# Optimization experiments

Hardware: AMD Instinct MI355X
Metric: run time of the kernel (lower is better)

The kernel has to match this reference:

```python
import jax, jax.numpy as jnp
import numpy as np

EPS = 1e-5
P = 3  # p_size
BW = 1.0  # bandwidth


def _instance_norm(x):
    # calc_mean_std: per (B,C) mean/std over spatial dims, unbiased var (torch default)
    b, c, h, w = x.shape
    flat = x.reshape(b, c, h * w)
    mean = flat.mean(-1)[:, :, None, None]
    std = jnp.sqrt(flat.var(-1, ddof=1) + EPS)[:, :, None, None]
    return (x - mean) / std


def _conv1x1(x, w, bias):
    # x: (B,C,H,W), w: (O,C), bias: (O,)
    return jnp.einsum('oc,bchw->bohw', w, x) + bias[None, :, None, None]


def _patches_scaled(x, scale):
    # ReflectionPad2d(1) + Unfold(3) -> (B, HW, C*9), torch layout (c slow, k fast),
    # with ContextAtten scale applied over the 9 kernel positions.
    b, c, h, w = x.shape
    pad = jnp.pad(x, ((0, 0), (0, 0), (1, 1), (1, 1)), mode='reflect')
    # (B,C,H,W,9)
    p9 = jnp.stack([pad[:, :, di:di + h, dj:dj + w]
                    for di in range(P) for dj in range(P)], axis=-1)
    p9 = p9 * scale  # broadcast over last (kernel) axis
    # -> (B,H,W,C,9) -> (B, HW, C*9)
    return p9.transpose(0, 2, 3, 1, 4).reshape(b, h * w, c * P * P)


def setup_inputs() -> dict:
    key = jax.random.key(0)
    ks = jax.random.split(key, 12)
    B, C, H, W = 2, 512, 64, 64
    IC = 256
    f32 = jnp.float32
    inp = {
        'content': jax.random.normal(ks[0], (B, C, H, W), f32),
        'style': jax.random.normal(ks[1], (B, C, H, W), f32),
        'fusion_style': jax.random.normal(ks[2], (B, C, H, W), f32),
        'theta_w': jax.random.normal(ks[3], (IC, C), f32) * np.sqrt(2.0 / C),
        'theta_b': jnp.zeros((IC,), f32),
        'phi_w': jax.random.normal(ks[4], (IC, C), f32) * np.sqrt(2.0 / C),
        'phi_b': jnp.zeros((IC,), f32),
        'g_w': jax.random.normal(ks[5], (IC, C), f32) * np.sqrt(2.0 / C),
        'g_b': jnp.zeros((IC,), f32),
        'W_w': jax.random.normal(ks[6], (C, IC), f32) * np.sqrt(2.0 / IC),
        'W_b': jnp.zeros((C,), f32),
        'scale': jnp.ones((P * P,), f32),
    }
    return inp


def reference(content, style, fusion_style, theta_w, theta_b, phi_w, phi_b,
              g_w, g_b, W_w, W_b, scale):
    B, C, H, W = content.shape
    IC = theta_w.shape[0]
    HW = H * W

    # g on fusion_style -> (B, HW, IC)
    g_s = _conv1x1(fusion_style, g_w, g_b).reshape(B, IC, HW).transpose(0, 2, 1)

    # instance-normalize content/style (normal=True path)
    xn = _instance_norm(content)
    sn = _instance_norm(style)

    theta_x = _conv1x1(xn, theta_w, theta_b)
    phi_s = _conv1x1(sn, phi_w, phi_b)

    theta_p = _patches_scaled(theta_x, scale)  # (B, HW, IC*9)
    phi_p = _patches_scaled(phi_s, scale)      # (B, HW, IC*9)

    f = jnp.einsum('blk,bmk->blm', theta_p, phi_p) * BW  # (B, HW, HW)
    f_div_C = jax.nn.softmax(f, axis=-1)

    y = jnp.einsum('blm,bmo->blo', f_div_C, g_s)  # (B, HW, IC)
    y = y.transpose(0, 2, 1).reshape(B, IC, H, W)
    W_y = _conv1x1(y, W_w, W_b)  # (B, C, H, W)
    # isTraining=True path: conf_map = 0
    return W_y
```

## Files before the change

### kernel.cpp

```cpp
#include <hip/hip_runtime.h>
#include <stdint.h>

typedef __attribute__((ext_vector_type(8))) __bf16 bf16x8;
typedef __attribute__((ext_vector_type(4))) float f32x4;
typedef __attribute__((ext_vector_type(4))) unsigned int uint4v;

__device__ __forceinline__ float bf2f(unsigned short u){
  unsigned int x = ((unsigned int)u) << 16;
  return __builtin_bit_cast(float, x);
}
__device__ __forceinline__ unsigned short f2bf(float f){
  unsigned int x = __builtin_bit_cast(unsigned int, f);
  x += 0x7FFFu + ((x >> 16) & 1u);
  return (unsigned short)(x >> 16);
}

#define OUT_PART 4
#define OUT_PARTH 5

template<int OM>
__global__ __launch_bounds__(256)
void gemm_bt(const unsigned short* __restrict__ A, int lda,
             const unsigned short* __restrict__ Bt, int ldb,
             int kchunk, void* __restrict__ Out, int ldo,
             size_t zStride, size_t aBatch, size_t bBatch,
             int sMask, int sShift)
{
  __shared__ uint4v AsmBuf[1024];
  __shared__ uint4v BsmBuf[1024];
  char* Asm = (char*)AsmBuf;
  char* Bsm = (char*)BsmBuf;

  const int tid  = threadIdx.x;
  const int lane = tid & 63;
  const int wave = tid >> 6;
  const int wy = wave >> 1, wx = wave & 1;
  const int lm = lane & 15, quad = lane >> 4;
  const int tileM = blockIdx.y * 128;
  const int tileN = blockIdx.x * 128;
  const int z = blockIdx.z;
  const int slice = z & sMask;
  const int batch = z >> sShift;

  A  += (size_t)slice*kchunk + (size_t)batch*aBatch;
  Bt += (size_t)slice*kchunk + (size_t)batch*bBatch;

  const int sr0 = tid >> 2, sc0 = tid & 3;
  const int sr1 = sr0 + 64;
  const size_t gA0 = (size_t)(tileM + sr0)*lda + ((sc0 ^ ((sr0 >> 1) & 3)) << 3);
  const size_t gA1 = (size_t)(tileM + sr1)*lda + ((sc0 ^ ((sr1 >> 1) & 3)) << 3);
  const size_t gB0 = (size_t)(tileN + sr0)*ldb + ((sc0 ^ ((sr0 >> 1) & 3)) << 3);
  const size_t gB1 = (size_t)(tileN + sr1)*ldb + ((sc0 ^ ((sr1 >> 1) & 3)) << 3);
  const int lOff0 = sr0*64 + sc0*16;
  const int lOff1 = sr1*64 + sc0*16;

  int aOff[4], bOff[4];
#pragma unroll
  for (int t = 0; t < 4; ++t){
    int ra = wy*64 + t*16 + lm;
    aOff[t] = ra*64 + ((quad ^ ((ra >> 1) & 3)) << 4);
    int rb = wx*64 + t*16 + lm;
    bOff[t] = rb*64 + ((quad ^ ((rb >> 1) & 3)) << 4);
  }

  f32x4 acc[4][4] = {};

  const int ksteps = kchunk >> 5;
  uint4v a0v = *(const uint4v*)(A + gA0);
  uint4v a1v = *(const uint4v*)(A + gA1);
  uint4v b0v = *(const uint4v*)(Bt + gB0);
  uint4v b1v = *(const uint4v*)(Bt + gB1);

  for (int kt = 0; kt < ksteps; ++kt){
    char* As = Asm + (kt & 1)*8192;
    char* Bs = Bsm + (kt & 1)*8192;
    *(uint4v*)(As + lOff0) = a0v;
    *(uint4v*)(As + lOff1) = a1v;
    *(uint4v*)(Bs + lOff0) = b0v;
    *(uint4v*)(Bs + lOff1) = b1v;
    __syncthreads();
    if (kt + 1 < ksteps){
      const unsigned short* Ak = A + (kt + 1)*32;
      const unsigned short* Bk = Bt + (kt + 1)*32;
      a0v = *(const uint4v*)(Ak + gA0);
      a1v = *(const uint4v*)(Ak + gA1);
      b0v = *(const uint4v*)(Bk + gB0);
      b1v = *(const uint4v*)(Bk + gB1);
    }
    bf16x8 af[4], bfr[4];
#pragma unroll
    for (int t = 0; t < 4; ++t){
      af[t]  = __builtin_bit_cast(bf16x8, *(const uint4v*)(As + aOff[t]));
      bfr[t] = __builtin_bit_cast(bf16x8, *(const uint4v*)(Bs + bOff[t]));
    }
#pragma unroll
    for (int tm = 0; tm < 4; ++tm)
#pragma unroll
      for (int tn = 0; tn < 4; ++tn)
        acc[tm][tn] = __builtin_amdgcn_mfma_f32_16x16x32_bf16(af[tm], bfr[tn], acc[tm][tn], 0, 0, 0);
  }

#pragma unroll
  for (int tm = 0; tm < 4; ++tm){
    const int rowb = tileM + wy*64 + tm*16 + quad*4;
#pragma unroll
    for (int tn = 0; tn < 4; ++tn){
      const int col = tileN + wx*64 + tn*16 + lm;
#pragma unroll
      for (int r = 0; r < 4; ++r){
        const float v = acc[tm][tn][r];
        const size_t idx = (size_t)z*zStride + (size_t)(rowb + r)*ldo + col;
        if (OM == OUT_PART) ((float*)Out)[idx] = v;
        else                ((unsigned short*)Out)[idx] = f2bf(v);
      }
    }
  }
}

template<int OM>
__global__ __launch_bounds__(256)
void gemm_wide(const unsigned short* __restrict__ A, int lda,
               const unsigned short* __restrict__ Bt, int ldb,
               int kchunk, void* __restrict__ Out, int ldo,
               size_t zStride, size_t aBatch, size_t bBatch,
               int sMask, int sShift)
{
  __shared__ uint4v AsmBuf[1024];
  __shared__ uint4v BsmBuf[2048];
  char* Asm = (char*)AsmBuf;
  char* Bsm = (char*)BsmBuf;

  const int tid  = threadIdx.x;
  const int lane = tid & 63;
  const int wave = tid >> 6;
  const int wy = wave >> 1, wx = wave & 1;
  const int lm = lane & 15, quad = lane >> 4;
  const int tileM = blockIdx.y * 128;
  const int tileN = blockIdx.x * 256;
  const int z = blockIdx.z;
  const int slice = z & sMask;
  const int batch = z >> sShift;

  A  += (size_t)slice*kchunk + (size_t)batch*aBatch;
  Bt += (size_t)slice*kchunk + (size_t)batch*bBatch;

  const int sr = tid >> 2, sc = tid & 3;
  size_t gA[2]; int lA[2];
  size_t gB[4]; int lB[4];
#pragma unroll
  for (int i = 0; i < 2; ++i){
    const int r = sr + 64*i;
    gA[i] = (size_t)(tileM + r)*lda + ((sc ^ ((r >> 1) & 3)) << 3);
    lA[i] = r*64 + sc*16;
  }
#pragma unroll
  for (int i = 0; i < 4; ++i){
    const int r = sr + 64*i;
    gB[i] = (size_t)(tileN + r)*ldb + ((sc ^ ((r >> 1) & 3)) << 3);
    lB[i] = r*64 + sc*16;
  }

  int aOff[4], bOff[8];
#pragma unroll
  for (int t = 0; t < 4; ++t){
    const int ra = wy*64 + t*16 + lm;
    aOff[t] = ra*64 + ((quad ^ ((ra >> 1) & 3)) << 4);
  }
#pragma unroll
  for (int t = 0; t < 8; ++t){
    const int rb = wx*128 + t*16 + lm;
    bOff[t] = rb*64 + ((quad ^ ((rb >> 1) & 3)) << 4);
  }

  f32x4 acc[4][8] = {};

  const int ksteps = kchunk >> 5;
  uint4v av[2], bv[4];
#pragma unroll
  for (int i = 0; i < 2; ++i) av[i] = *(const uint4v*)(A + gA[i]);
#pragma unroll
  for (int i = 0; i < 4; ++i) bv[i] = *(const uint4v*)(Bt + gB[i]);

  for (int kt = 0; kt < ksteps; ++kt){
    char* As = Asm + (kt & 1)*8192;
    char* Bs = Bsm + (kt & 1)*16384;
#pragma unroll
    for (int i = 0; i < 2; ++i) *(uint4v*)(As + lA[i]) = av[i];
#pragma unroll
    for (int i = 0; i < 4; ++i) *(uint4v*)(Bs + lB[i]) = bv[i];
    __syncthreads();
    if (kt + 1 < ksteps){
      const unsigned short* Ak = A + (kt + 1)*32;
      const unsigned short* Bk = Bt + (kt + 1)*32;
#pragma unroll
      for (int i = 0; i < 2; ++i) av[i] = *(const uint4v*)(Ak + gA[i]);
#pragma unroll
      for (int i = 0; i < 4; ++i) bv[i] = *(const uint4v*)(Bk + gB[i]);
    }
    bf16x8 af[4], bfr[8];
#pragma unroll
    for (int t = 0; t < 4; ++t)
      af[t] = __builtin_bit_cast(bf16x8, *(const uint4v*)(As + aOff[t]));
#pragma unroll
    for (int t = 0; t < 8; ++t)
      bfr[t] = __builtin_bit_cast(bf16x8, *(const uint4v*)(Bs + bOff[t]));
#pragma unroll
    for (int tm = 0; tm < 4; ++tm)
#pragma unroll
      for (int tn = 0; tn < 8; ++tn)
        acc[tm][tn] = __builtin_amdgcn_mfma_f32_16x16x32_bf16(af[tm], bfr[tn], acc[tm][tn], 0, 0, 0);
  }

#pragma unroll
  for (int tm = 0; tm < 4; ++tm){
    const int rowb = tileM + wy*64 + tm*16 + quad*4;
#pragma unroll
    for (int tn = 0; tn < 8; ++tn){
      const int col = tileN + wx*128 + tn*16 + lm;
#pragma unroll
      for (int r = 0; r < 4; ++r){
        const float v = acc[tm][tn][r];
        const size_t idx = (size_t)z*zStride + (size_t)(rowb + r)*ldo + col;
        if (OM == OUT_PART) ((float*)Out)[idx] = v;
        else                ((unsigned short*)Out)[idx] = f2bf(v);
      }
    }
  }
}

typedef const __attribute__((address_space(1))) unsigned int* gas1_t;
typedef __attribute__((address_space(3))) unsigned int* las3_t;
__device__ __forceinline__ void gload16(const void* g, void* l){
  __builtin_amdgcn_global_load_lds((gas1_t)g, (las3_t)l, 16, 0, 0);
}

__global__ __launch_bounds__(512)
void gemm_big256(const unsigned short* __restrict__ A, int lda,
                 const unsigned short* __restrict__ Bt, int ldb,
                 int K, float* __restrict__ Out, int ldo,
                 size_t aBatch, size_t bBatch, size_t oBatch)
{
  __shared__ char lds[65536];

  const int tid  = threadIdx.x;
  const int lane = tid & 63;
  const int wv   = tid >> 6;
  const int wy = wv >> 2, wx = wv & 3;
  const int lm = lane & 15, quad = lane >> 4;
  const int tileM = blockIdx.y * 256;
  const int tileN = blockIdx.x * 256;
  const int z = blockIdx.z;

  A   += (size_t)z*aBatch;
  Bt  += (size_t)z*bBatch;
  Out += (size_t)z*oBatch;

  const int srow  = tid >> 2;
  const int selem = (((tid & 3) ^ ((tid >> 3) & 3)) << 3);
  const size_t gAs  = (size_t)(tileM + srow)*lda + selem;
  const size_t gAs2 = gAs + (size_t)128*lda;
  const size_t gBs  = (size_t)(tileN + srow)*ldb + selem;
  const size_t gBs2 = gBs + (size_t)128*ldb;
  const int ldsSt = tid << 4;

  const int xq    = (quad ^ ((lm >> 1) & 3)) << 4;
  const int aBase = (wy*128 + lm)*64 + xq;
  const int bBase = (wx*64  + lm)*64 + xq;

  f32x4 acc[8][4] = {};
  const int nk = K >> 5;

  gload16(A  + gAs,  lds + ldsSt);
  gload16(A  + gAs2, lds + ldsSt + 8192);
  gload16(Bt + gBs,  lds + 16384 + ldsSt);
  gload16(Bt + gBs2, lds + 16384 + ldsSt + 8192);

  for (int kt = 0; kt < nk; ++kt){
    if (kt + 1 < nk){
      char* nbuf = lds + ((kt + 1) & 1)*32768;
      const unsigned short* Ak = A  + (kt + 1)*32;
      const unsigned short* Bk = Bt + (kt + 1)*32;
      gload16(Ak + gAs,  nbuf + ldsSt);
      gload16(Ak + gAs2, nbuf + ldsSt + 8192);
      gload16(Bk + gBs,  nbuf + 16384 + ldsSt);
      gload16(Bk + gBs2, nbuf + 16384 + ldsSt + 8192);
      asm volatile("s_waitcnt vmcnt(4)" ::: "memory");
    } else {
      asm volatile("s_waitcnt vmcnt(0)" ::: "memory");
    }
    __builtin_amdgcn_s_barrier();
    __builtin_amdgcn_sched_barrier(0);

    const char* As = lds + (kt & 1)*32768;
    const char* Bs = As + 16384;

    bf16x8 a[4], b[4];
#pragma unroll
    for (int n = 0; n < 4; ++n)
      b[n] = __builtin_bit_cast(bf16x8, *(const uint4v*)(Bs + bBase + n*1024));
#pragma unroll
    for (int m = 0; m < 4; ++m)
      a[m] = __builtin_bit_cast(bf16x8, *(const uint4v*)(As + aBase + m*1024));

    __builtin_amdgcn_s_barrier();
    __builtin_amdgcn_s_setprio(1);
#pragma unroll
    for (int m = 0; m < 4; ++m)
#pragma unroll
      for (int n = 0; n < 4; ++n)
        acc[m][n] = __builtin_amdgcn_mfma_f32_16x16x32_bf16(a[m], b[n], acc[m][n], 0, 0, 0);
    __builtin_amdgcn_s_setprio(0);
    __builtin_amdgcn_s_barrier();
    __builtin_amdgcn_sched_barrier(0);

#pragma unroll
    for (int m = 0; m < 4; ++m)
      a[m] = __builtin_bit_cast(bf16x8, *(const uint4v*)(As + aBase + (m + 4)*1024));
    __builtin_amdgcn_s_setprio(1);
#pragma unroll
    for (int m = 0; m < 4; ++m)
#pragma unroll
      for (int n = 0; n < 4; ++n)
        acc[m + 4][n] = __builtin_amdgcn_mfma_f32_16x16x32_bf16(a[m], b[n], acc[m + 4][n], 0, 0, 0);
    __builtin_amdgcn_s_setprio(0);
    __builtin_amdgcn_sched_barrier(0);
    __builtin_amdgcn_s_barrier();
    __builtin_amdgcn_sched_barrier(0);
    asm volatile("" ::: "memory");
  }

#pragma unroll
  for (int tm = 0; tm < 8; ++tm){
    const int rowb = tileM + wy*128 + tm*16 + quad*4;
#pragma unroll
    for (int tn = 0; tn < 4; ++tn){
      const int col = tileN + wx*64 + tn*16 + lm;
#pragma unroll
      for (int r = 0; r < 4; ++r)
        Out[(size_t)(rowb + r)*ldo + col] = acc[tm][tn][r];
    }
  }
}

__global__ __launch_bounds__(256)
void reduce_tp(const float* __restrict__ part,
               const float* __restrict__ tb, const float* __restrict__ pb,
               unsigned short* __restrict__ th, unsigned short* __restrict__ ph)
{
  const size_t i = (size_t)blockIdx.x*256 + threadIdx.x;
  const int which = (int)(i >> 21);
  const size_t j = i & 0x1FFFFFu;
  const int col = (int)(j & 255u);
  float v = 0.f;
#pragma unroll
  for (int s = 0; s < 4; ++s)
    v += part[(size_t)((which << 2) + s)*2097152 + j];
  v += (which ? pb : tb)[col];
  unsigned short hi = f2bf(v);
  unsigned short lo = f2bf(v - bf2f(hi));
  const size_t o = (j >> 8)*768 + col;
  unsigned short* O = which ? ph : th;
  const int dup = which ? 512 : 256;
  const int loo = which ? 256 : 512;
  O[o] = hi; O[o + dup] = hi; O[o + loo] = lo;
}

__global__ __launch_bounds__(256)
void reduce_g(const unsigned short* __restrict__ part,
              const float* __restrict__ gb, unsigned short* __restrict__ gs)
{
  const size_t i = (size_t)blockIdx.x*256 + threadIdx.x;
  float v = 0.f;
#pragma unroll
  for (int s = 0; s < 4; ++s) v += bf2f(part[(size_t)s*2097152 + i]);
  gs[i] = f2bf(v + gb[i >> 13]);
}

__global__ __launch_bounds__(256)
void reduce_y(const unsigned short* __restrict__ part,
              unsigned short* __restrict__ yb)
{
  const size_t i = (size_t)blockIdx.x*256 + threadIdx.x;
  const int b = (int)(i >> 20);
  const size_t j = i & 0xFFFFFu;
  float v = 0.f;
#pragma unroll
  for (int s = 0; s < 8; ++s)
    v += bf2f(part[(size_t)((b << 3) + s)*1048576 + j]);
  yb[i] = f2bf(v);
}

__global__ __launch_bounds__(256)
void reduce_w(const float* __restrict__ part, const float* __restrict__ wb,
              void* __restrict__ Out, const unsigned int* __restrict__ flagPtr)
{
  const size_t i = (size_t)blockIdx.x*256 + threadIdx.x;
  const int b = (int)(i >> 21);
  const size_t j = i & 0x1FFFFFu;
  float v = part[(size_t)(b << 1)*2097152 + j]
          + part[(size_t)((b << 1) | 1)*2097152 + j]
          + wb[(i >> 12) & 511u];
  if (flagPtr[0]) ((float*)Out)[i] = v;
  else            ((unsigned short*)Out)[i] = f2bf(v);
}

__global__ __launch_bounds__(256)
void detect_prep(const void* __restrict__ content,
                 const void* tb, const void* pb, const void* gb, const void* wb,
                 const void* sc,
                 unsigned int* __restrict__ flag, float* __restrict__ scale_c,
                 float* tb_c, float* pb_c, float* gb_c, float* wb_c)
{
  __shared__ int cnt;
  __shared__ unsigned int flg;
  const int tid = threadIdx.x;
  if (tid == 0) cnt = 0;
  __syncthreads();
  unsigned int w = ((const unsigned int*)content)[tid];
  int e = (w >> 23) & 0xFF;
  if (e >= 0x70 && e <= 0x8F) atomicAdd(&cnt, 1);
  __syncthreads();
  if (tid == 0){ flg = (cnt >= 128) ? 1u : 0u; flag[0] = flg; }
  __syncthreads();
  const unsigned int f = flg;
  auto rd = [&](const void* p, int i)->float{
    return f ? ((const float*)p)[i] : bf2f(((const unsigned short*)p)[i]);
  };
  if (tid < 9) scale_c[tid] = rd(sc, tid);
  tb_c[tid] = rd(tb, tid);
  pb_c[tid] = rd(pb, tid);
  gb_c[tid] = rd(gb, tid);
  wb_c[tid] = rd(wb, tid);
  wb_c[tid + 256] = rd(wb, tid + 256);
}

__global__ __launch_bounds__(256)
void conv_weights(const void* tw, const void* pw, const void* gw, const void* www,
                  const unsigned int* __restrict__ flagPtr,
                  unsigned short* __restrict__ wdup,
                  unsigned short* __restrict__ gwc,
                  unsigned short* __restrict__ wwc)
{
  const unsigned int fl = flagPtr[0];
  const int sec = blockIdx.y;
  const int idx = blockIdx.x*256 + threadIdx.x;
  auto rd = [&](const void* p, int i)->float{
    return fl ? ((const float*)p)[i] : bf2f(((const unsigned short*)p)[i]);
  };
  if (sec < 2){
    const void* w = sec ? pw : tw;
    const int o = idx >> 9, c = idx & 511;
    float v = rd(w, o*512 + c);
    unsigned short hi = f2bf(v);
    unsigned short lo = f2bf(v - bf2f(hi));
    unsigned short* base = wdup + (size_t)sec*256*1536 + o*1536;
    base[c] = hi; base[512 + c] = lo; base[1024 + c] = hi;
  } else if (sec == 2){
    const int o = idx >> 9, c = idx & 511;
    gwc[o*512 + c] = f2bf(rd(gw, o*512 + c));
  } else {
    const int o = idx >> 8, c = idx & 255;
    wwc[o*256 + c] = f2bf(rd(www, o*256 + c));
  }
}

__global__ __launch_bounds__(256)
void stats_all(const void* __restrict__ content, const void* __restrict__ style,
               const unsigned int* __restrict__ flagPtr,
               float* __restrict__ statsC, float* __restrict__ statsS)
{
  const unsigned int fl = flagPtr[0];
  const void* X = blockIdx.z ? style : content;
  float* stats = blockIdx.z ? statsS : statsC;
  const int bc = blockIdx.x;
  const int tid = threadIdx.x;
  float s = 0.f, q = 0.f;
  if (fl){
    const f32x4* row = (const f32x4*)((const float*)X + (size_t)bc*4096);
#pragma unroll
    for (int i = 0; i < 4; ++i){
      f32x4 v = row[tid + i*256];
#pragma unroll
      for (int j = 0; j < 4; ++j){ s += v[j]; q += v[j]*v[j]; }
    }
  } else {
    const uint4v* row = (const uint4v*)((const unsigned short*)X + (size_t)bc*4096);
#pragma unroll
    for (int i = 0; i < 2; ++i){
      uint4v u = row[tid + i*256];
#pragma unroll
      for (int j = 0; j < 4; ++j){
        float a = bf2f((unsigned short)(u[j] & 0xffffu));
        float b = bf2f((unsigned short)(u[j] >> 16));
        s += a + b; q += a*a + b*b;
      }
    }
  }
#pragma unroll
  for (int off = 32; off > 0; off >>= 1){
    s += __shfl_down(s, off);
    q += __shfl_down(q, off);
  }
  __shared__ float rs[4], rq[4];
  if ((tid & 63) == 0){ rs[tid >> 6] = s; rq[tid >> 6] = q; }
  __syncthreads();
  if (tid == 0){
    s = rs[0] + rs[1] + rs[2] + rs[3];
    q = rq[0] + rq[1] + rq[2] + rq[3];
    float mean = s * (1.0f/4096.0f);
    float var  = (q - 4096.0f*mean*mean) * (1.0f/4095.0f);
    stats[bc*2 + 0] = mean;
    stats[bc*2 + 1] = 1.0f / sqrtf(var + 1e-5f);
  }
}

__global__ __launch_bounds__(256)
void norm_all(const void* __restrict__ content, const void* __restrict__ style,
              const void* __restrict__ fusion,
              const float* __restrict__ statsC, const float* __restrict__ statsS,
              unsigned short* __restrict__ xn, unsigned short* __restrict__ sn,
              unsigned short* __restrict__ fst,
              const unsigned int* __restrict__ flagPtr)
{
  __shared__ float tile[64][65];
  const unsigned int fl = flagPtr[0];
  const int z = blockIdx.z;
  const int which = z >> 1;
  const int b  = z & 1;
  const int l0 = blockIdx.x * 64;
  const int c0 = blockIdx.y * 64;
  const int tid = threadIdx.x;
  const int tx = tid & 63, ty = tid >> 6;

  const void* X = which == 0 ? content : (which == 1 ? style : fusion);
#pragma unroll
  for (int p = 0; p < 16; ++p){
    const int cc = ty + p*4;
    const size_t src = ((size_t)b*512 + c0 + cc)*4096 + l0 + tx;
    tile[cc][tx] = fl ? ((const float*)X)[src]
                      : bf2f(((const unsigned short*)X)[src]);
  }
  __syncthreads();
  if (which < 2){
    const float* stats = which ? statsS : statsC;
    const float mean = stats[(b*512 + c0 + tx)*2 + 0];
    const float inv  = stats[(b*512 + c0 + tx)*2 + 1];
    unsigned short* Out = which ? sn : xn;
#pragma unroll
    for (int p = 0; p < 16; ++p){
      const int lj = ty + p*4;
      const float v = (tile[tx][lj] - mean) * inv;
      const size_t o = ((size_t)b*4096 + l0 + lj)*1536 + c0 + tx;
      const unsigned short hi = f2bf(v);
      Out[o] = hi;
      Out[o + 512] = hi;
      Out[o + 1024] = f2bf(v - bf2f(hi));
    }
  } else {
#pragma unroll
    for (int p = 0; p < 16; ++p){
      const int lj = ty + p*4;
      const size_t o = ((size_t)b*4096 + l0 + lj)*512 + c0 + tx;
      fst[o] = f2bf(tile[tx][lj]);
    }
  }
}

__global__ __launch_bounds__(256)
void softmax_rows(const float* __restrict__ Gbase, const float* __restrict__ scale_c,
                  unsigned short* __restrict__ Pbase)
{
  const int bb = blockIdx.x >> 12;
  const int l  = blockIdx.x & 4095;
  const float* G = Gbase + (size_t)bb*16777216;
  unsigned short* P = Pbase + (size_t)bb*16777216;
  const int yy = l >> 6, xx = l & 63;
  const int tid = threadIdx.x;

  float s2[9];
  const float* rowp[9];
#pragma unroll
  for (int di = 0; di < 3; ++di){
    int ry = yy + di - 1; ry = ry < 0 ? 1 : (ry > 63 ? 62 : ry);
#pragma unroll
    for (int dj = 0; dj < 3; ++dj){
      int rx = xx + dj - 1; rx = rx < 0 ? 1 : (rx > 63 ? 62 : rx);
      const int k = di*3 + dj;
      const float s = scale_c[k];
      s2[k] = s*s;
      rowp[k] = G + (size_t)(ry*64 + rx)*4096;
    }
  }

  float fv[16];
  float mx = -3.0e38f;
#pragma unroll
  for (int i = 0; i < 16; ++i){
    const int m = tid + i*256;
    const int my = m >> 6, mxo = m & 63;
    int cy[3], cx[3];
#pragma unroll
    for (int d = 0; d < 3; ++d){
      int t0 = my + d - 1;  cy[d] = (t0 < 0 ? 1 : (t0 > 63 ? 62 : t0))*64;
      int t1 = mxo + d - 1; cx[d] = (t1 < 0 ? 1 : (t1 > 63 ? 62 : t1));
    }
    float v = 0.f;
#pragma unroll
    for (int di = 0; di < 3; ++di)
#pragma unroll
      for (int dj = 0; dj < 3; ++dj)
        v = fmaf(s2[di*3+dj], rowp[di*3+dj][cy[di] + cx[dj]], v);
    fv[i] = v;
    mx = fmaxf(mx, v);
  }

  __shared__ float redA[4], redB[4];
#pragma unroll
  for (int off = 32; off > 0; off >>= 1) mx = fmaxf(mx, __shfl_down(mx, off));
  if ((tid & 63) == 0) redA[tid >> 6] = mx;
  __syncthreads();
  mx = fmaxf(fmaxf(redA[0], redA[1]), fmaxf(redA[2], redA[3]));

  float sum = 0.f;
#pragma unroll
  for (int i = 0; i < 16; ++i){ fv[i] = __expf(fv[i] - mx); sum += fv[i]; }
#pragma unroll
  for (int off = 32; off > 0; off >>= 1) sum += __shfl_down(sum, off);
  if ((tid & 63) == 0) redB[tid >> 6] = sum;
  __syncthreads();
  sum = redB[0] + redB[1] + redB[2] + redB[3];
  const float inv = 1.0f / sum;

  unsigned short* Prow = P + (size_t)l*4096;
#pragma unroll
  for (int i = 0; i < 16; ++i) Prow[tid + i*256] = f2bf(fv[i]*inv);
}

extern "C" void kernel_launch(void* const* d_in, const int* in_sizes, int n_in,
                              void* d_out, int out_size, void* d_ws, size_t ws_size,
                              hipStream_t stream)
{
  const void* content = d_in[0];
  const void* style   = d_in[1];
  const void* fusion  = d_in[2];
  const void* theta_w = d_in[3];
  const void* theta_b = d_in[4];
  const void* phi_w   = d_in[5];
  const void* phi_b   = d_in[6];
  const void* g_w     = d_in[7];
  const void* g_b     = d_in[8];
  const void* W_w     = d_in[9];
  const void* W_b     = d_in[10];
  const void* scale   = d_in[11];

  char* ws = (char*)d_ws;
  size_t off = 0;
  auto take = [&](size_t bytes)->char*{
    char* p = ws + off; off += (bytes + 255) & ~(size_t)255; return p;
  };

  unsigned int* flag  = (unsigned int*)take(256);
  float* scale_c      = (float*)take(256);
  float* tb_c         = (float*)take(1024);
  float* pb_c         = (float*)take(1024);
  float* gb_c         = (float*)take(1024);
  float* wb_c         = (float*)take(2048);
  float* statsC       = (float*)take(1024ull*2*4);
  float* statsS       = (float*)take(1024ull*2*4);
  unsigned short* wdup = (unsigned short*)take(2ull*256*1536*2);
  unsigned short* gwc  = (unsigned short*)take(256ull*512*2);
  unsigned short* wwc  = (unsigned short*)take(512ull*256*2);
  unsigned short* th   = (unsigned short*)take(8192ull*768*2);
  unsigned short* ph   = (unsigned short*)take(8192ull*768*2);
  unsigned short* gs   = (unsigned short*)take(256ull*8192*2);
  unsigned short* yb   = (unsigned short*)take(2ull*4096*256*2);
  float* G0            = (float*)take(4096ull*4096*4);
  float* G1            = (float*)take(4096ull*4096*4);
  char* unionC         = take(64ull*1024*1024);
  unsigned short* xn   = (unsigned short*)unionC;
  unsigned short* sn   = (unsigned short*)(unionC + 8192ull*1536*2);
  unsigned short* fst  = (unsigned short*)(unionC + 2ull*8192*1536*2);
  unsigned short* P    = (unsigned short*)unionC;

  float* partTP          = G0;
  unsigned short* partG  = (unsigned short*)G1;
  unsigned short* partY  = (unsigned short*)G0;
  float* partW           = G1;

  detect_prep<<<1, 256, 0, stream>>>(content, theta_b, phi_b, g_b, W_b, scale,
                                     flag, scale_c, tb_c, pb_c, gb_c, wb_c);
  conv_weights<<<dim3(512,4), 256, 0, stream>>>(theta_w, phi_w, g_w, W_w, flag,
                                                wdup, gwc, wwc);
  stats_all<<<dim3(1024,1,2), 256, 0, stream>>>(content, style, flag, statsC, statsS);
  norm_all<<<dim3(64,8,6), 256, 0, stream>>>(content, style, fusion,
                                             statsC, statsS, xn, sn, fst, flag);

  gemm_wide<OUT_PART><<<dim3(1,64,8), 256, 0, stream>>>(
      xn, 1536, wdup, 1536, 384, partTP, 256, 8192ull*256,
      8192ull*1536, 256ull*1536, 3, 2);
  reduce_tp<<<16384, 256, 0, stream>>>(partTP, tb_c, pb_c, th, ph);

  gemm_bt<OUT_PARTH><<<dim3(64,2,4), 256, 0, stream>>>(
      gwc, 512, fst, 512, 128, partG, 8192, 256ull*8192, 0, 0, 3, 2);
  reduce_g<<<8192, 256, 0, stream>>>(partG, gb_c, gs);

  gemm_big256<<<dim3(16,16,2), 512, 0, stream>>>(
      th, 768, ph, 768, 768, G0, 4096,
      4096ull*768, 4096ull*768, (size_t)(G1 - G0));

  softmax_rows<<<8192, 256, 0, stream>>>(G0, scale_c, P);

  gemm_wide<OUT_PARTH><<<dim3(1,32,16), 256, 0, stream>>>(
      P, 4096, gs, 8192, 512, partY, 256, 4096ull*256,
      16777216ull, 4096ull, 7, 3);
  reduce_y<<<8192, 256, 0, stream>>>(partY, yb);

  gemm_bt<OUT_PART><<<dim3(32,4,4), 256, 0, stream>>>(
      wwc, 256, yb, 256, 128, partW, 4096, 512ull*4096,
      0, 4096ull*256, 1, 1);
  reduce_w<<<16384, 256, 0, stream>>>(partW, wb_c, d_out, flag);
}
```

Baseline: 383.2 us.

## Deepen gemm_big256 K-tile to 64 with four-phase interleaved load/MFMA pipeline

```diff
diff --git a/kernel.cpp b/kernel.cpp
--- a/kernel.cpp
+++ b/kernel.cpp
@@ -234,13 +234,13 @@
   __builtin_amdgcn_global_load_lds((gas1_t)g, (las3_t)l, 16, 0, 0);
 }
 
-__global__ __launch_bounds__(512)
+__global__ __launch_bounds__(512, 2)
 void gemm_big256(const unsigned short* __restrict__ A, int lda,
                  const unsigned short* __restrict__ Bt, int ldb,
                  int K, float* __restrict__ Out, int ldo,
                  size_t aBatch, size_t bBatch, size_t oBatch)
 {
-  __shared__ char lds[65536];
+  __shared__ char lds[131072];
 
   const int tid  = threadIdx.x;
   const int lane = tid & 63;
@@ -255,78 +255,155 @@
   Bt  += (size_t)z*bBatch;
   Out += (size_t)z*oBatch;
 
-  const int srow  = tid >> 2;
-  const int selem = (((tid & 3) ^ ((tid >> 3) & 3)) << 3);
-  const size_t gAs  = (size_t)(tileM + srow)*lda + selem;
-  const size_t gAs2 = gAs + (size_t)128*lda;
-  const size_t gBs  = (size_t)(tileN + srow)*ldb + selem;
-  const size_t gBs2 = gBs + (size_t)128*ldb;
-  const int ldsSt = tid << 4;
-
-  const int xq    = (quad ^ ((lm >> 1) & 3)) << 4;
-  const int aBase = (wy*128 + lm)*64 + xq;
-  const int bBase = (wx*64  + lm)*64 + xq;
+  const int rp0 = tid >> 3;
+  const int cg  = (((tid & 7) ^ ((tid >> 3) & 7)) << 3);
+  const int dst = tid << 4;
+  const size_t eA0[2] = { (size_t)(tileM + rp0)*lda + cg,
+                          (size_t)(tileM + 128 + rp0)*lda + cg };
+  const size_t eA1[2] = { (size_t)(tileM + 64 + rp0)*lda + cg,
+                          (size_t)(tileM + 192 + rp0)*lda + cg };
+  const int rb0 = ((rp0 >> 5) << 6) + (rp0 & 31);
+  const int rb1 = (((rp0 + 64) >> 5) << 6) + ((rp0 + 64) & 31);
+  const size_t eB0[2] = { (size_t)(tileN + rb0)*ldb + cg,
+                          (size_t)(tileN + rb1)*ldb + cg };
+  const size_t eB1[2] = { (size_t)(tileN + rb0 + 32)*ldb + cg,
+                          (size_t)(tileN + rb1 + 32)*ldb + cg };
+
+  int aR[8], bR[4], csw[2];
+#pragma unroll
+  for (int m = 0; m < 8; ++m)
+    aR[m] = (((wy << 6) + ((m & 3) << 4) + ((m >> 2) << 7) + lm) << 7);
+#pragma unroll
+  for (int n = 0; n < 4; ++n)
+    bR[n] = (((wx << 5) + ((n & 1) << 4) + ((n >> 1) << 7) + lm) << 7);
+#pragma unroll
+  for (int kk = 0; kk < 2; ++kk)
+    csw[kk] = ((((kk << 2) + quad) ^ (lm & 7)) << 4);
 
   f32x4 acc[8][4] = {};
-  const int nk = K >> 5;
-
-  gload16(A  + gAs,  lds + ldsSt);
-  gload16(A  + gAs2, lds + ldsSt + 8192);
-  gload16(Bt + gBs,  lds + 16384 + ldsSt);
-  gload16(Bt + gBs2, lds + 16384 + ldsSt + 8192);
-
-  for (int kt = 0; kt < nk; ++kt){
-    if (kt + 1 < nk){
-      char* nbuf = lds + ((kt + 1) & 1)*32768;
-      const unsigned short* Ak = A  + (kt + 1)*32;
-      const unsigned short* Bk = Bt + (kt + 1)*32;
-      gload16(Ak + gAs,  nbuf + ldsSt);
-      gload16(Ak + gAs2, nbuf + ldsSt + 8192);
-      gload16(Bk + gBs,  nbuf + 16384 + ldsSt);
-      gload16(Bk + gBs2, nbuf + 16384 + ldsSt + 8192);
-      asm volatile("s_waitcnt vmcnt(4)" ::: "memory");
-    } else {
-      asm volatile("s_waitcnt vmcnt(0)" ::: "memory");
-    }
+  const int nt = K >> 6;
+
+  gload16(A  + eA0[0], lds + dst);
+  gload16(A  + eA0[1], lds + 8192 + dst);
+  gload16(Bt + eB0[0], lds + 32768 + dst);
+  gload16(Bt + eB0[1], lds + 32768 + 8192 + dst);
+  gload16(Bt + eB1[0], lds + 32768 + 16384 + dst);
+  gload16(Bt + eB1[1], lds + 32768 + 16384 + 8192 + dst);
+  gload16(A  + eA1[0], lds + 16384 + dst);
+  gload16(A  + eA1[1], lds + 16384 + 8192 + dst);
+  asm volatile("s_waitcnt vmcnt(4)" ::: "memory");
+  __builtin_amdgcn_s_barrier();
+  __builtin_amdgcn_sched_barrier(0);
+
+  for (int t = 0; t < nt; ++t){
+    const char* As = lds + (t & 1)*65536;
+    const char* Bs = As + 32768;
+    char* nxt = lds + ((t + 1) & 1)*65536;
+    const bool hn = (t + 1 < nt);
+    const unsigned short* An = A  + (size_t)(t + 1)*64;
+    const unsigned short* Bn = Bt + (size_t)(t + 1)*64;
+
+    bf16x8 aw[4][2], bw[4][2];
+
+#pragma unroll
+    for (int m = 0; m < 4; ++m)
+#pragma unroll
+      for (int kk = 0; kk < 2; ++kk)
+        aw[m][kk] = __builtin_bit_cast(bf16x8, *(const uint4v*)(As + aR[m] + csw[kk]));
+#pragma unroll
+    for (int n = 0; n < 2; ++n)
+#pragma unroll
+      for (int kk = 0; kk < 2; ++kk)
+        bw[n][kk] = __builtin_bit_cast(bf16x8, *(const uint4v*)(Bs + bR[n] + csw[kk]));
+    if (hn){
+      gload16(An + eA0[0], nxt + dst);
+      gload16(An + eA0[1], nxt + 8192 + dst);
+    }
+    __builtin_amdgcn_s_barrier();
+    asm volatile("s_waitcnt lgkmcnt(0)" ::: "memory");
+    __builtin_amdgcn_sched_barrier(0);
+    __builtin_amdgcn_s_setprio(1);
+#pragma unroll
+    for (int m = 0; m < 4; ++m)
+#pragma unroll
+      for (int n = 0; n < 2; ++n)
+#pragma unroll
+        for (int kk = 0; kk < 2; ++kk)
+          acc[m][n] = __builtin_amdgcn_mfma_f32_16x16x32_bf16(aw[m][kk], bw[n][kk], acc[m][n], 0, 0, 0);
+    __builtin_amdgcn_s_setprio(0);
+    if (hn) asm volatile("s_waitcnt vmcnt(4)" ::: "memory");
+    else    asm volatile("s_waitcnt vmcnt(2)" ::: "memory");
     __builtin_amdgcn_s_barrier();
     __builtin_amdgcn_sched_barrier(0);
 
-    const char* As = lds + (kt & 1)*32768;
-    const char* Bs = As + 16384;
-
-    bf16x8 a[4], b[4];
-#pragma unroll
-    for (int n = 0; n < 4; ++n)
-      b[n] = __builtin_bit_cast(bf16x8, *(const uint4v*)(Bs + bBase + n*1024));
+#pragma unroll
+    for (int n = 2; n < 4; ++n)
+#pragma unroll
+      for (int kk = 0; kk < 2; ++kk)
+        bw[n][kk] = __builtin_bit_cast(bf16x8, *(const uint4v*)(Bs + bR[n] + csw[kk]));
+    if (hn){
+      gload16(Bn + eB0[0], nxt + 32768 + dst);
+      gload16(Bn + eB0[1], nxt + 32768 + 8192 + dst);
+    }
+    __builtin_amdgcn_s_barrier();
+    asm volatile("s_waitcnt lgkmcnt(0)" ::: "memory");
+    __builtin_amdgcn_sched_barrier(0);
+    __builtin_amdgcn_s_setprio(1);
 #pragma unroll
     for (int m = 0; m < 4; ++m)
-      a[m] = __builtin_bit_cast(bf16x8, *(const uint4v*)(As + aBase + m*1024));
-
+#pragma unroll
+      for (int n = 2; n < 4; ++n)
+#pragma unroll
+        for (int kk = 0; kk < 2; ++kk)
+          acc[m][n] = __builtin_amdgcn_mfma_f32_16x16x32_bf16(aw[m][kk], bw[n][kk], acc[m][n], 0, 0, 0);
+    __builtin_amdgcn_s_setprio(0);
+    if (hn) asm volatile("s_waitcnt vmcnt(4)" ::: "memory");
+    else    asm volatile("s_waitcnt vmcnt(0)" ::: "memory");
     __builtin_amdgcn_s_barrier();
+    __builtin_amdgcn_sched_barrier(0);
+
+#pragma unroll
+    for (int m = 0; m < 4; ++m)
+#pragma unroll
+      for (int kk = 0; kk < 2; ++kk)
+        aw[m][kk] = __builtin_bit_cast(bf16x8, *(const uint4v*)(As + aR[m + 4] + csw[kk]));
+    if (hn){
+      gload16(Bn + eB1[0], nxt + 32768 + 16384 + dst);
+      gload16(Bn + eB1[1], nxt + 32768 + 16384 + 8192 + dst);
+    }
+    __builtin_amdgcn_s_barrier();
+    asm volatile("s_waitcnt lgkmcnt(0)" ::: "memory");
+    __builtin_amdgcn_sched_barrier(0);
     __builtin_amdgcn_s_setprio(1);
 #pragma unroll
     for (int m = 0; m < 4; ++m)
 #pragma unroll
-      for (int n = 0; n < 4; ++n)
-        acc[m][n] = __builtin_amdgcn_mfma_f32_16x16x32_bf16(a[m], b[n], acc[m][n], 0, 0, 0);
+      for (int n = 2; n < 4; ++n)
+#pragma unroll
+        for (int kk = 0; kk < 2; ++kk)
+          acc[m + 4][n] = __builtin_amdgcn_mfma_f32_16x16x32_bf16(aw[m][kk], bw[n][kk], acc[m + 4][n], 0, 0, 0);
     __builtin_amdgcn_s_setprio(0);
     __builtin_amdgcn_s_barrier();
     __builtin_amdgcn_sched_barrier(0);
 
-#pragma unroll
-    for (int m = 0; m < 4; ++m)
-      a[m] = __builtin_bit_cast(bf16x8, *(const uint4v*)(As + aBase + (m + 4)*1024));
-    __builtin_amdgcn_s_setprio(1);
-#pragma unroll
-    for (int m = 0; m < 4; ++m)
-#pragma unroll
-      for (int n = 0; n < 4; ++n)
-        acc[m + 4][n] = __builtin_amdgcn_mfma_f32_16x16x32_bf16(a[m], b[n], acc[m + 4][n], 0, 0, 0);
-    __builtin_amdgcn_s_setprio(0);
-    __builtin_amdgcn_sched_barrier(0);
+    if (hn){
+      gload16(An + eA1[0], nxt + 16384 + dst);
+      gload16(An + eA1[1], nxt + 16384 + 8192 + dst);
+    }
     __builtin_amdgcn_s_barrier();
     __builtin_amdgcn_sched_barrier(0);
-    asm volatile("" ::: "memory");
+    __builtin_amdgcn_s_setprio(1);
+#pragma unroll
+    for (int m = 0; m < 4; ++m)
+#pragma unroll
+      for (int n = 0; n < 2; ++n)
+#pragma unroll
+        for (int kk = 0; kk < 2; ++kk)
+          acc[m + 4][n] = __builtin_amdgcn_mfma_f32_16x16x32_bf16(aw[m][kk], bw[n][kk], acc[m + 4][n], 0, 0, 0);
+    __builtin_amdgcn_s_setprio(0);
+    if (hn) asm volatile("s_waitcnt vmcnt(4)" ::: "memory");
+    __builtin_amdgcn_s_barrier();
+    __builtin_amdgcn_sched_barrier(0);
   }
 
 #pragma unroll
```

New measurement: 376.0 us. About the same (-1.9%).
